# Optimization experiments

Hardware: AMD Instinct MI355X
Metric: run time of the kernel (lower is better)

## Reference

```python
import jax, jax.numpy as jnp
import numpy as np

N_NODES = 100000


def setup_inputs() -> dict:
    key = jax.random.key(0)
    ks = jax.random.split(key, 8)
    IN, HID, OUT = 128, 128, 64
    E = 1600000
    x = jax.random.normal(ks[0], (N_NODES, IN), dtype=jnp.float32)
    edge_index = jax.random.randint(ks[1], (2, E), 0, N_NODES, dtype=jnp.int64)
    # PyG SAGEConv params: lin_l (applied to aggregated neighbors, with bias),
    # lin_r (root weight, no bias).
    def lin(k, fi, fo):
        return jax.random.normal(k, (fi, fo), dtype=jnp.float32) / np.sqrt(fi)
    Wl0 = lin(ks[2], IN, HID)
    bl0 = jnp.zeros((HID,), dtype=jnp.float32)
    Wr0 = lin(ks[3], IN, HID)
    Wl1 = lin(ks[4], HID, OUT)
    bl1 = jnp.zeros((OUT,), dtype=jnp.float32)
    Wr1 = lin(ks[5], HID, OUT)
    return {"x": x, "edge_index": edge_index,
            "Wl0": Wl0, "bl0": bl0, "Wr0": Wr0,
            "Wl1": Wl1, "bl1": bl1, "Wr1": Wr1}


def _sage_conv(h, src, dst, Wl, bl, Wr):
    # mean aggregation of source features onto target nodes
    summed = jax.ops.segment_sum(h[src], dst, num_segments=N_NODES)  # [N, d]
    cnt = jax.ops.segment_sum(jnp.ones((src.shape[0], 1), h.dtype), dst,
                              num_segments=N_NODES)                  # [N, 1]
    agg = summed / jnp.maximum(cnt, 1.0)
    return agg @ Wl + bl + h @ Wr


def reference(x, edge_index, Wl0, bl0, Wr0, Wl1, bl1, Wr1):
    src, dst = edge_index[0], edge_index[1]
    h = jax.nn.relu(_sage_conv(x, src, dst, Wl0, bl0, Wr0))
    # dropout is identity in eval mode (training=False)
    return _sage_conv(h, src, dst, Wl1, bl1, Wr1)
```

## Files before the change

kernel.cpp:

```cpp
#include <hip/hip_runtime.h>


typedef short short8 __attribute__((ext_vector_type(8)));
typedef float f32x4 __attribute__((ext_vector_type(4)));
typedef float f32x2 __attribute__((ext_vector_type(2)));

#define NBUCK 782
#define BCAP  3072
#define EPB   2048

static __device__ __forceinline__ unsigned short f2bf(float f) {
    union { float f; unsigned u; } c; c.f = f;
    unsigned u = c.u + 0x7fffu + ((c.u >> 16) & 1u);
    return (unsigned short)(u >> 16);
}
static __device__ __forceinline__ float bf2f(unsigned short b) {
    union { unsigned u; float f; } c; c.u = ((unsigned)b) << 16;
    return c.f;
}
static __device__ __forceinline__ float bf2f_s(short b) {
    return bf2f((unsigned short)b);
}

static __device__ __forceinline__ unsigned char f2fp8(float x) {
    union { float f; unsigned u; } c; c.f = x;
    unsigned s = (c.u >> 24) & 0x80u;
    float a = __builtin_fabsf(x);
    if (a < 0.015625f) {
        int m = (int)rintf(a * 512.0f);
        return (unsigned char)(s | (unsigned)m);
    }
    unsigned u = c.u + 0x7ffffu + ((c.u >> 20) & 1u);
    int e = (int)((u >> 23) & 0xff) - 120;
    unsigned m = (u >> 20) & 7u;
    if (e > 15) { e = 15; m = 6; }
    return (unsigned char)(s | (unsigned)(e << 3) | m);
}

static __device__ __forceinline__ void acc_fp8x4(unsigned w, float* a) {
#if __has_builtin(__builtin_amdgcn_cvt_pk_f32_fp8)
    f32x2 lo = __builtin_amdgcn_cvt_pk_f32_fp8((int)w, false);
    f32x2 hi = __builtin_amdgcn_cvt_pk_f32_fp8((int)w, true);
    a[0] += lo[0]; a[1] += lo[1]; a[2] += hi[0]; a[3] += hi[1];
#else
    #pragma unroll
    for (int j = 0; j < 4; ++j) {
        unsigned b = (w >> (8 * j)) & 0xffu;
        union { unsigned u; float f; } c;
        c.u = ((b & 0x80u) << 24) | ((b & 0x7fu) << 20);
        a[j] += c.f * 0x1p120f;
    }
#endif
}
static __device__ __forceinline__ void acc_row16(uint4 w, float* a) {
    acc_fp8x4(w.x, a + 0);  acc_fp8x4(w.y, a + 4);
    acc_fp8x4(w.z, a + 8);  acc_fp8x4(w.w, a + 12);
}

__global__ __launch_bounds__(256) void k_pack2(const float* __restrict__ Wl0,
        const float* __restrict__ Wr0, const float* __restrict__ Wl1,
        const float* __restrict__ Wr1, unsigned short* __restrict__ Wp0,
        unsigned short* __restrict__ Wp1) {
    int tid = blockIdx.x * 256 + threadIdx.x;
    const float *WA, *WB; int CA; unsigned short* Wp;
    if (tid < 4096) {
        WA = Wl0; WB = Wr0; CA = 128; Wp = Wp0;
    } else {
        tid -= 4096;
        if (tid >= 2048) return;
        WA = Wl1; WB = Wr1; CA = 64; Wp = Wp1;
    }
    int lane = tid & 63, kk = (tid >> 6) & 3, tg = tid >> 8;
    int l15 = lane & 15, quad = lane >> 4;
    int c = tg * 16 + l15;
    const float* W = (c < CA) ? WA : WB;
    int cc = (c < CA) ? c : c - CA;
    short8 v;
    #pragma unroll
    for (int j = 0; j < 8; ++j) {
        int k = kk * 32 + quad * 8 + j;
        v[j] = (short)f2bf(W[(size_t)k * CA + cc]);
    }
    *(short8*)(Wp + (size_t)tid * 8) = v;
}

__global__ __launch_bounds__(256) void k_gemm0_bucket(
        const float* __restrict__ X, const unsigned short* __restrict__ Wp,
        unsigned char* __restrict__ P0, unsigned short* __restrict__ Q0, int Nrows,
        const int* __restrict__ src, const int* __restrict__ dst,
        int* __restrict__ cursor, int* __restrict__ bregion,
        int E, int bucketBlocks) {
    const int t = threadIdx.x;
    if ((int)blockIdx.x >= bucketBlocks) {
        const int wave = t >> 6, lane = t & 63;
        const int quad = lane >> 4, l15 = lane & 15;
        const int row0 = (blockIdx.x - bucketBlocks) * 32;
        const int c0w = wave * 64;
        f32x4 acc[2][4];
        #pragma unroll
        for (int mt = 0; mt < 2; ++mt)
            #pragma unroll
            for (int tt = 0; tt < 4; ++tt) acc[mt][tt] = (f32x4){0.f, 0.f, 0.f, 0.f};
        #pragma unroll
        for (int kk = 0; kk < 4; ++kk) {
            const int k0 = kk * 32 + quad * 8;
            short8 a[2];
            #pragma unroll
            for (int mt = 0; mt < 2; ++mt) {
                int row = row0 + mt * 16 + l15;
                if (row > Nrows - 1) row = Nrows - 1;
                const float* xp = X + (size_t)row * 128 + k0;
                float4 f0 = *(const float4*)xp;
                float4 f1 = *(const float4*)(xp + 4);
                short8 v;
                v[0] = (short)f2bf(f0.x); v[1] = (short)f2bf(f0.y);
                v[2] = (short)f2bf(f0.z); v[3] = (short)f2bf(f0.w);
                v[4] = (short)f2bf(f1.x); v[5] = (short)f2bf(f1.y);
                v[6] = (short)f2bf(f1.z); v[7] = (short)f2bf(f1.w);
                a[mt] = v;
            }
            short8 b[4];
            #pragma unroll
            for (int tt = 0; tt < 4; ++tt) {
                int tg = (c0w >> 4) + tt;
                b[tt] = *(const short8*)(Wp + ((size_t)(tg * 4 + kk) * 64 + lane) * 8);
            }
            #pragma unroll
            for (int mt = 0; mt < 2; ++mt)
                #pragma unroll
                for (int tt = 0; tt < 4; ++tt)
                    acc[mt][tt] = __builtin_amdgcn_mfma_f32_16x16x32_bf16(
                        a[mt], b[tt], acc[mt][tt], 0, 0, 0);
        }
        #pragma unroll
        for (int mt = 0; mt < 2; ++mt)
            #pragma unroll
            for (int r = 0; r < 4; ++r) {
                int row = row0 + mt * 16 + quad * 4 + r;
                if (row < Nrows) {
                    if (c0w < 128) {
                        #pragma unroll
                        for (int tt = 0; tt < 4; ++tt)
                            P0[(size_t)row * 128 + c0w + tt * 16 + l15] =
                                f2fp8(acc[mt][tt][r]);
                    } else {
                        #pragma unroll
                        for (int tt = 0; tt < 4; ++tt)
                            Q0[(size_t)row * 128 + (c0w - 128) + tt * 16 + l15] =
                                f2bf(acc[mt][tt][r]);
                    }
                }
            }
        return;
    }
    __shared__ int hist[NBUCK];
    __shared__ int basel[NBUCK];
    int bid = blockIdx.x;
    for (int i = t; i < NBUCK; i += 256) hist[i] = 0;
    __syncthreads();
    int e0 = bid * EPB + t * 8;
    if (e0 + 8 <= E) {
        #pragma unroll
        for (int q = 0; q < 2; ++q) {
            int4 v = *(const int4*)(dst + e0 + q * 4);
            atomicAdd(&hist[v.x >> 7], 1);
            atomicAdd(&hist[v.y >> 7], 1);
            atomicAdd(&hist[v.z >> 7], 1);
            atomicAdd(&hist[v.w >> 7], 1);
        }
    } else {
        for (int j = 0; j < 8; ++j)
            if (e0 + j < E) atomicAdd(&hist[dst[e0 + j] >> 7], 1);
    }
    __syncthreads();
    for (int i = t; i < NBUCK; i += 256) {
        int c = hist[i];
        basel[i] = (c > 0) ? atomicAdd(&cursor[i], c) : 0;
    }
    __syncthreads();
    for (int i = t; i < NBUCK; i += 256) hist[i] = 0;
    __syncthreads();
    if (e0 + 8 <= E) {
        #pragma unroll
        for (int q = 0; q < 2; ++q) {
            int4 dv = *(const int4*)(dst + e0 + q * 4);
            int4 sv = *(const int4*)(src + e0 + q * 4);
            int dd[4] = {dv.x, dv.y, dv.z, dv.w};
            int ss[4] = {sv.x, sv.y, sv.z, sv.w};
            #pragma unroll
            for (int j = 0; j < 4; ++j) {
                int b = dd[j] >> 7;
                int r = atomicAdd(&hist[b], 1);
                bregion[(size_t)b * BCAP + basel[b] + r] = ss[j] | ((dd[j] & 127) << 20);
            }
        }
    } else {
        for (int j = 0; j < 8; ++j) {
            if (e0 + j < E) {
                int dd = dst[e0 + j], ss = src[e0 + j];
                int b = dd >> 7;
                int r = atomicAdd(&hist[b], 1);
                bregion[(size_t)b * BCAP + basel[b] + r] = ss | ((dd & 127) << 20);
            }
        }
    }
}

__global__ __launch_bounds__(256) void k_csr(const int* __restrict__ cursor,
                                             const int* __restrict__ bregion,
                                             int* __restrict__ rowptr,
                                             int* __restrict__ csr, int Nn) {
    __shared__ int words[BCAP];
    __shared__ int hist[128], sc[128], rank[128];
    __shared__ int red[256];
    int b = blockIdx.x, t = threadIdx.x;
    int part = 0;
    for (int i = t; i < b; i += 256) part += cursor[i];
    red[t] = part;
    if (t < 128) { hist[t] = 0; rank[t] = 0; }
    __syncthreads();
    #pragma unroll
    for (int off = 128; off > 0; off >>= 1) {
        if (t < off) red[t] += red[t + off];
        __syncthreads();
    }
    int gbase = red[0];
    int cnt = cursor[b];
    for (int i = t; i < cnt; i += 256) {
        int w = bregion[(size_t)b * BCAP + i];
        words[i] = w;
        atomicAdd(&hist[w >> 20], 1);
    }
    __syncthreads();
    if (t < 128) sc[t] = hist[t];
    __syncthreads();
    #pragma unroll
    for (int off = 1; off < 128; off <<= 1) {
        int x = 0;
        if (t < 128 && t >= off) x = sc[t - off];
        __syncthreads();
        if (t < 128) sc[t] += x;
        __syncthreads();
    }
    if (t < 128) sc[t] -= hist[t];
    __syncthreads();
    if (t < 128) {
        int node = b * 128 + t;
        if (node <= Nn) rowptr[node] = gbase + sc[t];
    }
    for (int i = t; i < cnt; i += 256) {
        int w = words[i];
        int d7 = w >> 20;
        int r = atomicAdd(&rank[d7], 1);
        csr[gbase + sc[d7] + r] = w & 0xFFFFF;
    }
}

__global__ __launch_bounds__(256) void k_agg0_gemm1(
        const unsigned char* __restrict__ P0,
        const unsigned short* __restrict__ Q0,
        const int* __restrict__ rowptr, const int* __restrict__ csr,
        const float* __restrict__ bl0,
        const unsigned short* __restrict__ Wp,
        unsigned char* __restrict__ P1, unsigned short* __restrict__ Q1,
        int Nn) {
    __shared__ unsigned short ht[32 * 128];
    const int t = threadIdx.x;
    const int wave = t >> 6, lane = t & 63;
    {
        int g = lane >> 3, l7 = lane & 7;
        int nloc = wave * 8 + g;
        int n = blockIdx.x * 32 + nloc;
        bool live = (n < Nn);
        int st = 0, dg = 0;
        if (live) { st = rowptr[n]; dg = rowptr[n + 1] - st; }
        float acc[16] = {};
        int e = 0;
        for (; e + 2 <= dg; e += 2) {
            int s0 = csr[st + e];
            int s1 = csr[st + e + 1];
            uint4 w0 = *(const uint4*)(P0 + (size_t)s0 * 128 + l7 * 16);
            uint4 w1 = *(const uint4*)(P0 + (size_t)s1 * 128 + l7 * 16);
            acc_row16(w0, acc);
            acc_row16(w1, acc);
        }
        if (e < dg) {
            int s0 = csr[st + e];
            uint4 w0 = *(const uint4*)(P0 + (size_t)s0 * 128 + l7 * 16);
            acc_row16(w0, acc);
        }
        short8 o0 = (short8){0,0,0,0,0,0,0,0}, o1 = o0;
        if (live) {
            float inv = 1.f / fmaxf((float)dg, 1.f);
            short8 q0 = *(const short8*)(Q0 + (size_t)n * 128 + l7 * 16);
            short8 q1 = *(const short8*)(Q0 + (size_t)n * 128 + l7 * 16 + 8);
            float bb[16];
            *(float4*)(bb + 0)  = *(const float4*)(bl0 + l7 * 16);
            *(float4*)(bb + 4)  = *(const float4*)(bl0 + l7 * 16 + 4);
            *(float4*)(bb + 8)  = *(const float4*)(bl0 + l7 * 16 + 8);
            *(float4*)(bb + 12) = *(const float4*)(bl0 + l7 * 16 + 12);
            #pragma unroll
            for (int j = 0; j < 8; ++j)
                o0[j] = (short)f2bf(fmaxf(acc[j] * inv + bb[j] + bf2f_s(q0[j]), 0.f));
            #pragma unroll
            for (int j = 0; j < 8; ++j)
                o1[j] = (short)f2bf(fmaxf(acc[8 + j] * inv + bb[8 + j] + bf2f_s(q1[j]), 0.f));
        }
        unsigned sw = (unsigned)(nloc & 7) << 4;
        char* base = (char*)ht + nloc * 256;
        *(short8*)(base + (((unsigned)(l7 * 32)) ^ sw)) = o0;
        *(short8*)(base + (((unsigned)(l7 * 32 + 16)) ^ sw)) = o1;
    }
    __syncthreads();
    const int quad = lane >> 4, l15 = lane & 15;
    const int row0 = blockIdx.x * 32;
    const int c0w = wave * 32;
    f32x4 acc[2][2];
    #pragma unroll
    for (int mt = 0; mt < 2; ++mt)
        #pragma unroll
        for (int tt = 0; tt < 2; ++tt) acc[mt][tt] = (f32x4){0.f, 0.f, 0.f, 0.f};
    #pragma unroll
    for (int kk = 0; kk < 4; ++kk) {
        short8 a[2];
        #pragma unroll
        for (int mt = 0; mt < 2; ++mt) {
            int row = mt * 16 + l15;
            const char* p = (const char*)ht + row * 256 +
                (((unsigned)(kk * 64 + quad * 16)) ^ ((unsigned)(row & 7) << 4));
            a[mt] = *(const short8*)p;
        }
        short8 b[2];
        #pragma unroll
        for (int tt = 0; tt < 2; ++tt) {
            int tg = (c0w >> 4) + tt;
            b[tt] = *(const short8*)(Wp + ((size_t)(tg * 4 + kk) * 64 + lane) * 8);
        }
        #pragma unroll
        for (int mt = 0; mt < 2; ++mt)
            #pragma unroll
            for (int tt = 0; tt < 2; ++tt)
                acc[mt][tt] = __builtin_amdgcn_mfma_f32_16x16x32_bf16(
                    a[mt], b[tt], acc[mt][tt], 0, 0, 0);
    }
    #pragma unroll
    for (int mt = 0; mt < 2; ++mt)
        #pragma unroll
        for (int r = 0; r < 4; ++r) {
            int row = row0 + mt * 16 + quad * 4 + r;
            if (row < Nn) {
                if (c0w < 64) {
                    #pragma unroll
                    for (int tt = 0; tt < 2; ++tt)
                        P1[(size_t)row * 64 + c0w + tt * 16 + l15] =
                            f2fp8(acc[mt][tt][r]);
                } else {
                    #pragma unroll
                    for (int tt = 0; tt < 2; ++tt)
                        Q1[(size_t)row * 64 + (c0w - 64) + tt * 16 + l15] =
                            f2bf(acc[mt][tt][r]);
                }
            }
        }
}

__global__ __launch_bounds__(256) void k_agg1(const unsigned char* __restrict__ P1,
                                              const unsigned short* __restrict__ Q1,
                                              const int* __restrict__ rowptr,
                                              const int* __restrict__ csr,
                                              const float* __restrict__ bl1,
                                              float* __restrict__ out, int Nn) {
    int wave = threadIdx.x >> 6, lane = threadIdx.x & 63;
    int g = lane >> 2, l3 = lane & 3;
    int n = (blockIdx.x * 4 + wave) * 16 + g;
    bool live = (n < Nn);
    int st = 0, dg = 0;
    if (live) { st = rowptr[n]; dg = rowptr[n + 1] - st; }
    float acc[16] = {};
    int e = 0;
    for (; e + 2 <= dg; e += 2) {
        int s0 = csr[st + e];
        int s1 = csr[st + e + 1];
        uint4 w0 = *(const uint4*)(P1 + (size_t)s0 * 64 + l3 * 16);
        uint4 w1 = *(const uint4*)(P1 + (size_t)s1 * 64 + l3 * 16);
        acc_row16(w0, acc);
        acc_row16(w1, acc);
    }
    if (e < dg) {
        int s0 = csr[st + e];
        uint4 w0 = *(const uint4*)(P1 + (size_t)s0 * 64 + l3 * 16);
        acc_row16(w0, acc);
    }
    if (live) {
        float inv = 1.f / fmaxf((float)dg, 1.f);
        short8 q0 = *(const short8*)(Q1 + (size_t)n * 64 + l3 * 16);
        short8 q1 = *(const short8*)(Q1 + (size_t)n * 64 + l3 * 16 + 8);
        float bb[16];
        *(float4*)(bb + 0)  = *(const float4*)(bl1 + l3 * 16);
        *(float4*)(bb + 4)  = *(const float4*)(bl1 + l3 * 16 + 4);
        *(float4*)(bb + 8)  = *(const float4*)(bl1 + l3 * 16 + 8);
        *(float4*)(bb + 12) = *(const float4*)(bl1 + l3 * 16 + 12);
        float4 o[4];
        #pragma unroll
        for (int j = 0; j < 8; ++j)
            ((float*)o)[j] = acc[j] * inv + bb[j] + bf2f_s(q0[j]);
        #pragma unroll
        for (int j = 0; j < 8; ++j)
            ((float*)o)[8 + j] = acc[8 + j] * inv + bb[8 + j] + bf2f_s(q1[j]);
        #pragma unroll
        for (int q = 0; q < 4; ++q)
            *(float4*)(out + (size_t)n * 64 + l3 * 16 + q * 4) = o[q];
    }
}

extern "C" void kernel_launch(void* const* d_in, const int* in_sizes, int n_in,
                              void* d_out, int out_size, void* d_ws, size_t ws_size,
                              hipStream_t stream) {
    const float* x   = (const float*)d_in[0];
    const int* eidx  = (const int*)d_in[1];
    const float* Wl0 = (const float*)d_in[2];
    const float* bl0 = (const float*)d_in[3];
    const float* Wr0 = (const float*)d_in[4];
    const float* Wl1 = (const float*)d_in[5];
    const float* bl1 = (const float*)d_in[6];
    const float* Wr1 = (const float*)d_in[7];
    float* out = (float*)d_out;

    const int N = in_sizes[0] / 128;
    const int E = in_sizes[1] / 2;
    const int* src = eidx;
    const int* dst = eidx + E;

    int* rowptr  = (int*)d_ws;
    int* cursor  = rowptr + (N + 4);
    int* bregion = cursor + 784;
    int* csr     = bregion + (size_t)NBUCK * BCAP;
    unsigned short* Wp0 = (unsigned short*)(csr + E);
    unsigned short* Wp1 = Wp0 + 32768;
    unsigned char*  P0  = (unsigned char*)(Wp1 + 16384);
    unsigned short* Q0  = (unsigned short*)(P0 + (size_t)N * 128);
    unsigned short* h   = Q0 + (size_t)N * 128;
    unsigned char*  P1  = (unsigned char*)(h + (size_t)N * 128);
    unsigned short* Q1  = (unsigned short*)(P1 + (size_t)N * 64);

    hipMemsetAsync(cursor, 0, NBUCK * sizeof(int), stream);

    k_pack2<<<24, 256, 0, stream>>>(Wl0, Wr0, Wl1, Wr1, Wp0, Wp1);

    int gemmBlocks = (N + 31) / 32;
    int nbb = (E + EPB - 1) / EPB;
    k_gemm0_bucket<<<gemmBlocks + nbb, 256, 0, stream>>>(
        x, Wp0, P0, Q0, N, src, dst, cursor, bregion, E, nbb);
    k_csr<<<NBUCK, 256, 0, stream>>>(cursor, bregion, rowptr, csr, N);

    k_agg0_gemm1<<<(N + 31) / 32, 256, 0, stream>>>(
        P0, Q0, rowptr, csr, bl0, Wp1, P1, Q1, N);
    k_agg1<<<(N + 63) / 64, 256, 0, stream>>>(P1, Q1, rowptr, csr, bl1, out, N);
}
```

Baseline: 305.0 us.

## Replace bucketed CSR build with degree count, global scan, and atomic scatter

Replaces the two-pass bucket sort (a block-local histogram into 128-node buckets, then a per-bucket shared-memory sort in k_csr) with a standard CSR build. The new build counts per-node degrees with global atomics fused into the first GEMM launch, runs a three-kernel prefix scan, then scatters edges with per-node global atomics. This drops the bucket staging buffer and its second pass over the edges. In exchange it adds more kernel launches and 3.2M global atomics on 100k counters. The scatter order within a row becomes nondeterministic, and csr writes are random rather than coalesced per bucket.

```diff
diff --git a/kernel.cpp b/kernel.cpp
--- a/kernel.cpp
+++ b/kernel.cpp
@@ -5,9 +5,8 @@
 typedef float f32x4 __attribute__((ext_vector_type(4)));
 typedef float f32x2 __attribute__((ext_vector_type(2)));
 
-#define NBUCK 782
-#define BCAP  3072
-#define EPB   2048
+#define EPB   8192
+#define NCH   392
 
 static __device__ __forceinline__ unsigned short f2bf(float f) {
     union { float f; unsigned u; } c; c.f = f;
@@ -84,175 +83,164 @@
     *(short8*)(Wp + (size_t)tid * 8) = v;
 }
 
-__global__ __launch_bounds__(256) void k_gemm0_bucket(
+__global__ __launch_bounds__(256) void k_gemm0_deg(
         const float* __restrict__ X, const unsigned short* __restrict__ Wp,
         unsigned char* __restrict__ P0, unsigned short* __restrict__ Q0, int Nrows,
-        const int* __restrict__ src, const int* __restrict__ dst,
-        int* __restrict__ cursor, int* __restrict__ bregion,
-        int E, int bucketBlocks) {
+        const int* __restrict__ dst, int* __restrict__ deg,
+        int E, int degBlocks) {
     const int t = threadIdx.x;
-    if ((int)blockIdx.x >= bucketBlocks) {
-        const int wave = t >> 6, lane = t & 63;
-        const int quad = lane >> 4, l15 = lane & 15;
-        const int row0 = (blockIdx.x - bucketBlocks) * 32;
-        const int c0w = wave * 64;
-        f32x4 acc[2][4];
+    if ((int)blockIdx.x < degBlocks) {
+        int e0 = blockIdx.x * EPB + t * 32;
+        if (e0 + 32 <= E) {
+            #pragma unroll
+            for (int q = 0; q < 8; ++q) {
+                int4 v = *(const int4*)(dst + e0 + q * 4);
+                atomicAdd(&deg[v.x], 1);
+                atomicAdd(&deg[v.y], 1);
+                atomicAdd(&deg[v.z], 1);
+                atomicAdd(&deg[v.w], 1);
+            }
+        } else {
+            for (int j = 0; j < 32; ++j)
+                if (e0 + j < E) atomicAdd(&deg[dst[e0 + j]], 1);
+        }
+        return;
+    }
+    const int wave = t >> 6, lane = t & 63;
+    const int quad = lane >> 4, l15 = lane & 15;
+    const int row0 = (blockIdx.x - degBlocks) * 32;
+    const int c0w = wave * 64;
+    f32x4 acc[2][4];
+    #pragma unroll
+    for (int mt = 0; mt < 2; ++mt)
+        #pragma unroll
+        for (int tt = 0; tt < 4; ++tt) acc[mt][tt] = (f32x4){0.f, 0.f, 0.f, 0.f};
+    #pragma unroll
+    for (int kk = 0; kk < 4; ++kk) {
+        const int k0 = kk * 32 + quad * 8;
+        short8 a[2];
+        #pragma unroll
+        for (int mt = 0; mt < 2; ++mt) {
+            int row = row0 + mt * 16 + l15;
+            if (row > Nrows - 1) row = Nrows - 1;
+            const float* xp = X + (size_t)row * 128 + k0;
+            float4 f0 = *(const float4*)xp;
+            float4 f1 = *(const float4*)(xp + 4);
+            short8 v;
+            v[0] = (short)f2bf(f0.x); v[1] = (short)f2bf(f0.y);
+            v[2] = (short)f2bf(f0.z); v[3] = (short)f2bf(f0.w);
+            v[4] = (short)f2bf(f1.x); v[5] = (short)f2bf(f1.y);
+            v[6] = (short)f2bf(f1.z); v[7] = (short)f2bf(f1.w);
+            a[mt] = v;
+        }
+        short8 b[4];
+        #pragma unroll
+        for (int tt = 0; tt < 4; ++tt) {
+            int tg = (c0w >> 4) + tt;
+            b[tt] = *(const short8*)(Wp + ((size_t)(tg * 4 + kk) * 64 + lane) * 8);
+        }
         #pragma unroll
         for (int mt = 0; mt < 2; ++mt)
             #pragma unroll
-            for (int tt = 0; tt < 4; ++tt) acc[mt][tt] = (f32x4){0.f, 0.f, 0.f, 0.f};
-        #pragma unroll
-        for (int kk = 0; kk < 4; ++kk) {
-            const int k0 = kk * 32 + quad * 8;
-            short8 a[2];
-            #pragma unroll
-            for (int mt = 0; mt < 2; ++mt) {
-                int row = row0 + mt * 16 + l15;
-                if (row > Nrows - 1) row = Nrows - 1;
-                const float* xp = X + (size_t)row * 128 + k0;
-                float4 f0 = *(const float4*)xp;
-                float4 f1 = *(const float4*)(xp + 4);
-                short8 v;
-                v[0] = (short)f2bf(f0.x); v[1] = (short)f2bf(f0.y);
-                v[2] = (short)f2bf(f0.z); v[3] = (short)f2bf(f0.w);
-                v[4] = (short)f2bf(f1.x); v[5] = (short)f2bf(f1.y);
-                v[6] = (short)f2bf(f1.z); v[7] = (short)f2bf(f1.w);
-                a[mt] = v;
-            }
-            short8 b[4];
-            #pragma unroll
-            for (int tt = 0; tt < 4; ++tt) {
-                int tg = (c0w >> 4) + tt;
-                b[tt] = *(const short8*)(Wp + ((size_t)(tg * 4 + kk) * 64 + lane) * 8);
-            }
-            #pragma unroll
-            for (int mt = 0; mt < 2; ++mt)
-                #pragma unroll
-                for (int tt = 0; tt < 4; ++tt)
-                    acc[mt][tt] = __builtin_amdgcn_mfma_f32_16x16x32_bf16(
-                        a[mt], b[tt], acc[mt][tt], 0, 0, 0);
-        }
-        #pragma unroll
-        for (int mt = 0; mt < 2; ++mt)
-            #pragma unroll
-            for (int r = 0; r < 4; ++r) {
-                int row = row0 + mt * 16 + quad * 4 + r;
-                if (row < Nrows) {
-                    if (c0w < 128) {
-                        #pragma unroll
-                        for (int tt = 0; tt < 4; ++tt)
-                            P0[(size_t)row * 128 + c0w + tt * 16 + l15] =
-                                f2fp8(acc[mt][tt][r]);
-                    } else {
-                        #pragma unroll
-                        for (int tt = 0; tt < 4; ++tt)
-                            Q0[(size_t)row * 128 + (c0w - 128) + tt * 16 + l15] =
-                                f2bf(acc[mt][tt][r]);
-                    }
+            for (int tt = 0; tt < 4; ++tt)
+                acc[mt][tt] = __builtin_amdgcn_mfma_f32_16x16x32_bf16(
+                    a[mt], b[tt], acc[mt][tt], 0, 0, 0);
+    }
+    #pragma unroll
+    for (int mt = 0; mt < 2; ++mt)
+        #pragma unroll
+        for (int r = 0; r < 4; ++r) {
+            int row = row0 + mt * 16 + quad * 4 + r;
+            if (row < Nrows) {
+                if (c0w < 128) {
+                    #pragma unroll
+                    for (int tt = 0; tt < 4; ++tt)
+                        P0[(size_t)row * 128 + c0w + tt * 16 + l15] =
+                            f2fp8(acc[mt][tt][r]);
+                } else {
+                    #pragma unroll
+                    for (int tt = 0; tt < 4; ++tt)
+                        Q0[(size_t)row * 128 + (c0w - 128) + tt * 16 + l15] =
+                            f2bf(acc[mt][tt][r]);
                 }
             }
-        return;
-    }
-    __shared__ int hist[NBUCK];
-    __shared__ int basel[NBUCK];
-    int bid = blockIdx.x;
-    for (int i = t; i < NBUCK; i += 256) hist[i] = 0;
-    __syncthreads();
-    int e0 = bid * EPB + t * 8;
-    if (e0 + 8 <= E) {
-        #pragma unroll
-        for (int q = 0; q < 2; ++q) {
-            int4 v = *(const int4*)(dst + e0 + q * 4);
-            atomicAdd(&hist[v.x >> 7], 1);
-            atomicAdd(&hist[v.y >> 7], 1);
-            atomicAdd(&hist[v.z >> 7], 1);
-            atomicAdd(&hist[v.w >> 7], 1);
-        }
-    } else {
-        for (int j = 0; j < 8; ++j)
-            if (e0 + j < E) atomicAdd(&hist[dst[e0 + j] >> 7], 1);
-    }
-    __syncthreads();
-    for (int i = t; i < NBUCK; i += 256) {
-        int c = hist[i];
-        basel[i] = (c > 0) ? atomicAdd(&cursor[i], c) : 0;
-    }
-    __syncthreads();
-    for (int i = t; i < NBUCK; i += 256) hist[i] = 0;
-    __syncthreads();
-    if (e0 + 8 <= E) {
-        #pragma unroll
-        for (int q = 0; q < 2; ++q) {
-            int4 dv = *(const int4*)(dst + e0 + q * 4);
-            int4 sv = *(const int4*)(src + e0 + q * 4);
-            int dd[4] = {dv.x, dv.y, dv.z, dv.w};
-            int ss[4] = {sv.x, sv.y, sv.z, sv.w};
-            #pragma unroll
-            for (int j = 0; j < 4; ++j) {
-                int b = dd[j] >> 7;
-                int r = atomicAdd(&hist[b], 1);
-                bregion[(size_t)b * BCAP + basel[b] + r] = ss[j] | ((dd[j] & 127) << 20);
-            }
-        }
-    } else {
-        for (int j = 0; j < 8; ++j) {
-            if (e0 + j < E) {
-                int dd = dst[e0 + j], ss = src[e0 + j];
-                int b = dd >> 7;
-                int r = atomicAdd(&hist[b], 1);
-                bregion[(size_t)b * BCAP + basel[b] + r] = ss | ((dd & 127) << 20);
-            }
-        }
-    }
-}
-
-__global__ __launch_bounds__(256) void k_csr(const int* __restrict__ cursor,
-                                             const int* __restrict__ bregion,
-                                             int* __restrict__ rowptr,
-                                             int* __restrict__ csr, int Nn) {
-    __shared__ int words[BCAP];
-    __shared__ int hist[128], sc[128], rank[128];
+        }
+}
+
+__global__ __launch_bounds__(256) void k_scan_part(const int* __restrict__ deg,
+                                                   int* __restrict__ part) {
     __shared__ int red[256];
-    int b = blockIdx.x, t = threadIdx.x;
-    int part = 0;
-    for (int i = t; i < b; i += 256) part += cursor[i];
-    red[t] = part;
-    if (t < 128) { hist[t] = 0; rank[t] = 0; }
+    int t = threadIdx.x;
+    red[t] = deg[blockIdx.x * 256 + t];
     __syncthreads();
     #pragma unroll
     for (int off = 128; off > 0; off >>= 1) {
         if (t < off) red[t] += red[t + off];
         __syncthreads();
     }
-    int gbase = red[0];
-    int cnt = cursor[b];
-    for (int i = t; i < cnt; i += 256) {
-        int w = bregion[(size_t)b * BCAP + i];
-        words[i] = w;
-        atomicAdd(&hist[w >> 20], 1);
-    }
+    if (t == 0) part[blockIdx.x] = red[0];
+}
+
+__global__ __launch_bounds__(512) void k_scan_top(int* __restrict__ part, int nch) {
+    __shared__ int s[512];
+    int t = threadIdx.x;
+    int v = (t < nch) ? part[t] : 0;
+    s[t] = v;
     __syncthreads();
-    if (t < 128) sc[t] = hist[t];
+    #pragma unroll
+    for (int off = 1; off < 512; off <<= 1) {
+        int x = (t >= off) ? s[t - off] : 0;
+        __syncthreads();
+        s[t] += x;
+        __syncthreads();
+    }
+    if (t < nch) part[t] = s[t] - v;
+}
+
+__global__ __launch_bounds__(256) void k_scan_apply(const int* __restrict__ deg,
+                                                    const int* __restrict__ part,
+                                                    int* __restrict__ rowptr,
+                                                    int* __restrict__ cur, int Nn) {
+    __shared__ int s[256];
+    int t = threadIdx.x;
+    int idx = blockIdx.x * 256 + t;
+    int v = deg[idx];
+    s[t] = v;
     __syncthreads();
     #pragma unroll
-    for (int off = 1; off < 128; off <<= 1) {
-        int x = 0;
-        if (t < 128 && t >= off) x = sc[t - off];
+    for (int off = 1; off < 256; off <<= 1) {
+        int x = (t >= off) ? s[t - off] : 0;
         __syncthreads();
-        if (t < 128) sc[t] += x;
+        s[t] += x;
         __syncthreads();
     }
-    if (t < 128) sc[t] -= hist[t];
-    __syncthreads();
-    if (t < 128) {
-        int node = b * 128 + t;
-        if (node <= Nn) rowptr[node] = gbase + sc[t];
-    }
-    for (int i = t; i < cnt; i += 256) {
-        int w = words[i];
-        int d7 = w >> 20;
-        int r = atomicAdd(&rank[d7], 1);
-        csr[gbase + sc[d7] + r] = w & 0xFFFFF;
+    int excl = part[blockIdx.x] + s[t] - v;
+    if (idx <= Nn) { rowptr[idx] = excl; cur[idx] = excl; }
+}
+
+__global__ __launch_bounds__(256) void k_scatter(const int* __restrict__ src,
+                                                 const int* __restrict__ dst,
+                                                 int* __restrict__ cur,
+                                                 int* __restrict__ csr, int E) {
+    int t = threadIdx.x;
+    int e0 = blockIdx.x * EPB + t * 32;
+    if (e0 + 32 <= E) {
+        #pragma unroll
+        for (int q = 0; q < 8; ++q) {
+            int4 dv = *(const int4*)(dst + e0 + q * 4);
+            int4 sv = *(const int4*)(src + e0 + q * 4);
+            int p;
+            p = atomicAdd(&cur[dv.x], 1); csr[p] = sv.x;
+            p = atomicAdd(&cur[dv.y], 1); csr[p] = sv.y;
+            p = atomicAdd(&cur[dv.z], 1); csr[p] = sv.z;
+            p = atomicAdd(&cur[dv.w], 1); csr[p] = sv.w;
+        }
+    } else {
+        for (int j = 0; j < 32; ++j)
+            if (e0 + j < E) {
+                int p = atomicAdd(&cur[dst[e0 + j]], 1);
+                csr[p] = src[e0 + j];
+            }
     }
 }
 
@@ -430,28 +418,32 @@
     const int E = in_sizes[1] / 2;
     const int* src = eidx;
     const int* dst = eidx + E;
+    const int NS = NCH * 256;
 
     int* rowptr  = (int*)d_ws;
-    int* cursor  = rowptr + (N + 4);
-    int* bregion = cursor + 784;
-    int* csr     = bregion + (size_t)NBUCK * BCAP;
+    int* cur     = rowptr + (N + 8);
+    int* deg     = cur + (N + 8);
+    int* part    = deg + NS;
+    int* csr     = part + 512;
     unsigned short* Wp0 = (unsigned short*)(csr + E);
     unsigned short* Wp1 = Wp0 + 32768;
     unsigned char*  P0  = (unsigned char*)(Wp1 + 16384);
     unsigned short* Q0  = (unsigned short*)(P0 + (size_t)N * 128);
-    unsigned short* h   = Q0 + (size_t)N * 128;
-    unsigned char*  P1  = (unsigned char*)(h + (size_t)N * 128);
+    unsigned char*  P1  = (unsigned char*)(Q0 + (size_t)N * 128);
     unsigned short* Q1  = (unsigned short*)(P1 + (size_t)N * 64);
 
-    hipMemsetAsync(cursor, 0, NBUCK * sizeof(int), stream);
+    hipMemsetAsync(deg, 0, NS * sizeof(int), stream);
 
     k_pack2<<<24, 256, 0, stream>>>(Wl0, Wr0, Wl1, Wr1, Wp0, Wp1);
 
     int gemmBlocks = (N + 31) / 32;
     int nbb = (E + EPB - 1) / EPB;
-    k_gemm0_bucket<<<gemmBlocks + nbb, 256, 0, stream>>>(
-        x, Wp0, P0, Q0, N, src, dst, cursor, bregion, E, nbb);
-    k_csr<<<NBUCK, 256, 0, stream>>>(cursor, bregion, rowptr, csr, N);
+    k_gemm0_deg<<<nbb + gemmBlocks, 256, 0, stream>>>(
+        x, Wp0, P0, Q0, N, dst, deg, E, nbb);
+    k_scan_part<<<NCH, 256, 0, stream>>>(deg, part);
+    k_scan_top<<<1, 512, 0, stream>>>(part, NCH);
+    k_scan_apply<<<NCH, 256, 0, stream>>>(deg, part, rowptr, cur, N);
+    k_scatter<<<nbb, 256, 0, stream>>>(src, dst, cur, csr, E);
 
     k_agg0_gemm1<<<(N + 31) / 32, 256, 0, stream>>>(
         P0, Q0, rowptr, csr, bl0, Wp1, P1, Q1, N);
```

Result: slower. 380.7 us (+24.8%).
